# Kernel optimization log

Hardware: AMD Instinct MI355X
Metric: run time of the kernel (lower is better)

The kernel has to match this reference:

```python
import jax, jax.numpy as jnp
import numpy as np

N_NODES = 100000
N_EDGES = 1600000
D = 128


def gcn_conv(x, src, dst, ew, W, b, num_nodes):
    """PyG GCNConv: self-loops (weight 1), symmetric deg^{-1/2} normalization,
    linear transform (no bias) then scatter-add aggregation at dst, bias after."""
    loop = jnp.arange(num_nodes)
    s = jnp.concatenate([src, loop])
    d = jnp.concatenate([dst, loop])
    w = jnp.concatenate([ew, jnp.ones((num_nodes,), dtype=x.dtype)])
    deg = jax.ops.segment_sum(w, d, num_segments=num_nodes)
    dinv = jnp.where(deg > 0, jax.lax.rsqrt(deg), 0.0).astype(x.dtype)
    norm = dinv[s] * w * dinv[d]                      # [E+N]
    h = x @ W                                          # [N, out]
    msgs = h[s] * norm[:, None]                        # [E+N, out]
    return jax.ops.segment_sum(msgs, d, num_segments=num_nodes) + b


def setup_inputs() -> dict:
    key = jax.random.key(0)
    ks = jax.random.split(key, 7)
    x = jax.random.normal(ks[0], (N_NODES, D), dtype=jnp.float32)
    edge_index = jax.random.randint(ks[1], (2, N_EDGES), 0, N_NODES, dtype=jnp.int64)
    edge_weight = jax.random.uniform(ks[2], (N_EDGES,), dtype=jnp.float32)
    scale = 1.0 / np.sqrt(D)
    W1 = jax.random.normal(ks[3], (D, D), dtype=jnp.float32) * scale
    b1 = jax.random.normal(ks[4], (D,), dtype=jnp.float32) * 0.01
    W2 = jax.random.normal(ks[5], (D, D), dtype=jnp.float32) * scale
    b2 = jax.random.normal(ks[6], (D,), dtype=jnp.float32) * 0.01
    return {"x": x, "edge_index": edge_index, "edge_weight": edge_weight,
            "W1": W1, "b1": b1, "W2": W2, "b2": b2}


def reference(x, edge_index, edge_weight, W1, b1, W2, b2):
    src, dst = edge_index[0], edge_index[1]
    n = x.shape[0]
    h = gcn_conv(x, src, dst, edge_weight, W1, b1, n)
    h = jax.nn.relu(h)
    h = gcn_conv(h, src, dst, edge_weight, W2, b2, n)
    return jax.nn.relu(h)
```

## Files before the change

### kernel.cpp

```cpp
#include <hip/hip_runtime.h>

#define D 128
#define CAP 64
#define NCELL 391
#define BN2 256
#define CELLCAP 4608
#define BCAP 20
#define ABLK 512

typedef __attribute__((ext_vector_type(8))) short bf16x8;
typedef __attribute__((ext_vector_type(4))) float f32x4;

__device__ __forceinline__ ushort f2bf(float f) {
    uint u = __float_as_uint(f);
    return (ushort)((u + 0x7FFFu + ((u >> 16) & 1u)) >> 16);
}

__global__ __launch_bounds__(256) void k_prep(const float* __restrict__ W1,
                                              const float* __restrict__ W2,
                                              ushort* __restrict__ Wt1,
                                              ushort* __restrict__ Wt2,
                                              int* scnt) {
    int i = blockIdx.x * 256 + threadIdx.x;
    if (i < NCELL) scnt[i] = 0;
    if (i < 2 * D * D) {
        const float* W = (i < D * D) ? W1 : W2;
        ushort* Wt     = (i < D * D) ? Wt1 : Wt2;
        int j = i & (D * D - 1);
        int k = j >> 7, nn = j & 127;
        Wt[nn * D + k] = f2bf(W[k * D + nn]);
    }
}

__global__ __launch_bounds__(256) void k_bin(const int* __restrict__ src,
                                             const int* __restrict__ dst,
                                             const float* __restrict__ ew,
                                             int* scnt,
                                             uint2* __restrict__ rec, int nE, int epb) {
    __shared__ uint2 lrec[NCELL * BCAP];
    __shared__ int   bcnt[NCELL];
    __shared__ int   gbase[NCELL];
    const int tid = threadIdx.x;

    for (int i = tid; i < NCELL; i += 256) bcnt[i] = 0;
    __syncthreads();

    int e0 = blockIdx.x * epb;
    int e1 = min(e0 + epb, nE);
    for (int e = e0 + tid; e < e1; e += 256) {
        int d = dst[e];
        uint q = (uint)__float2int_rn(ew[e] * 32767.0f);
        uint2 r = make_uint2(((uint)src[e] << 15) | q, (uint)(d & (BN2 - 1)));
        int cell = d >> 8;
        int p = atomicAdd(&bcnt[cell], 1);
        if (p < BCAP) {
            lrec[cell * BCAP + p] = r;
        } else {
            int gp = atomicAdd(&scnt[cell], 1);
            if (gp < CELLCAP) rec[(size_t)cell * CELLCAP + gp] = r;
        }
    }
    __syncthreads();

    const int offs = (blockIdx.x * 97) % NCELL;

    for (int i = tid; i < NCELL; i += 256) {
        int cell = i + offs; if (cell >= NCELL) cell -= NCELL;
        int c = min(bcnt[cell], BCAP);
        gbase[cell] = (c > 0) ? atomicAdd(&scnt[cell], c) : 0;
    }
    __syncthreads();

    const int wave = tid >> 6, lane = tid & 63;
    for (int i = wave; i < NCELL; i += 4) {
        int cell = i + offs; if (cell >= NCELL) cell -= NCELL;
        int c = min(bcnt[cell], BCAP);
        if (lane < c)
            rec[(size_t)cell * CELLCAP + gbase[cell] + lane] = lrec[cell * BCAP + lane];
    }
}

__global__ __launch_bounds__(256) void k_build(const uint2* __restrict__ rec,
                                               const int* __restrict__ scnt,
                                               uint* __restrict__ bucket,
                                               int* __restrict__ cnt,
                                               float* __restrict__ dinv, int n) {
    __shared__ uint rows[BN2 * (CAP + 1)];
    __shared__ int  lcnt[BN2];
    const int tid = threadIdx.x;
    const int b   = blockIdx.x;

    lcnt[tid] = 0;
    __syncthreads();

    int c = min(scnt[b], CELLCAP);
    for (int i = tid; i < c; i += 256) {
        uint2 r = rec[(size_t)b * CELLCAP + i];
        int nl = (int)r.y;
        int p = atomicAdd(&lcnt[nl], 1);
        if (p < CAP) rows[nl * (CAP + 1) + p] = r.x;
    }
    __syncthreads();

    {
        int node = b * BN2 + tid;
        if (node < n) {
            int cc = min(lcnt[tid], CAP);
            float wsum = 0.f;
            for (int i = 0; i < cc; ++i)
                wsum += (float)(rows[tid * (CAP + 1) + i] & 32767u);
            dinv[node] = rsqrtf(1.0f + wsum * (1.0f / 32767.0f));
            cnt[node]  = cc;
        }
    }
    __syncthreads();

    for (int i = tid; i < BN2 * CAP; i += 256) {
        int nl = i >> 6, sl = i & (CAP - 1);
        int node = b * BN2 + nl;
        if (node < n) bucket[(size_t)node * CAP + sl] = rows[nl * (CAP + 1) + sl];
    }
}

template <bool IN_BF16>
__global__ __launch_bounds__(256) void k_gemm(const void* __restrict__ Xv,
                                              const ushort* __restrict__ Wt,
                                              ushort* __restrict__ H, int n) {
    __shared__ ushort Xs[64][136];
    __shared__ ushort Ws[128][136];
    const int tid  = threadIdx.x;
    const int row0 = blockIdx.x * 64;

#pragma unroll
    for (int p = 0; p < 8; ++p) {
        int f = (p * 256 + tid) * 8;
        int nn = f >> 7, kk = f & 127;
        *(uint4*)(&Ws[nn][kk]) = *(const uint4*)(Wt + f);
    }
    if (IN_BF16) {
        const ushort* X = (const ushort*)Xv;
#pragma unroll
        for (int p = 0; p < 4; ++p) {
            int f = (p * 256 + tid) * 8;
            int r = f >> 7, kk = f & 127;
            uint4 v = {0u, 0u, 0u, 0u};
            if (row0 + r < n) v = *(const uint4*)(X + (size_t)(row0 + r) * D + kk);
            *(uint4*)(&Xs[r][kk]) = v;
        }
    } else {
        const float* X = (const float*)Xv;
#pragma unroll
        for (int p = 0; p < 8; ++p) {
            int f = (p * 256 + tid) * 4;
            int r = f >> 7, kk = f & 127;
            float4 v = {0.f, 0.f, 0.f, 0.f};
            if (row0 + r < n) v = *(const float4*)(X + (size_t)(row0 + r) * D + kk);
            ushort4 o;
            o.x = f2bf(v.x); o.y = f2bf(v.y); o.z = f2bf(v.z); o.w = f2bf(v.w);
            *(ushort4*)(&Xs[r][kk]) = o;
        }
    }
    __syncthreads();

    const int lane = tid & 63;
    const int wave = tid >> 6;
    const int m    = lane & 15;
    const int quad = lane >> 4;
    const int rw   = wave * 16;

    f32x4 acc[8] = {};
#pragma unroll
    for (int kt = 0; kt < 4; ++kt) {
        int k0 = kt * 32 + quad * 8;
        bf16x8 a = *(const bf16x8*)(&Xs[rw + m][k0]);
#pragma unroll
        for (int t = 0; t < 8; ++t) {
            bf16x8 b = *(const bf16x8*)(&Ws[t * 16 + m][k0]);
            acc[t] = __builtin_amdgcn_mfma_f32_16x16x32_bf16(a, b, acc[t], 0, 0, 0);
        }
    }

#pragma unroll
    for (int t = 0; t < 8; ++t) {
#pragma unroll
        for (int r = 0; r < 4; ++r) {
            int row = row0 + rw + quad * 4 + r;
            if (row < n) H[(size_t)row * D + t * 16 + m] = f2bf(acc[t][r]);
        }
    }
}

template <bool OUT_BF16>
__global__ __launch_bounds__(256) void k_agg(const ushort* __restrict__ H,
                                             const int* __restrict__ cnt,
                                             const uint* __restrict__ bucket,
                                             const float* __restrict__ dinv,
                                             const float* __restrict__ bias,
                                             void* __restrict__ outv, int n) {
    int node = blockIdx.x * 4 + (threadIdx.x >> 6);
    if (node >= n) return;
    int lane = threadIdx.x & 63;
    const uint* Hu = (const uint*)H;
    const uint* row = bucket + (size_t)node * CAP;

    float di = dinv[node];
    float c0 = di * (1.0f / 32767.0f);
    uint hs = Hu[(size_t)node * 64 + lane];
    float accx = __uint_as_float(hs << 16) * (di * di);
    float accy = __uint_as_float(hs & 0xFFFF0000u) * (di * di);

    int c = cnt[node];
    int j = 0;
    for (; j + 3 < c; j += 4) {
        uint p0 = row[j],     p1 = row[j + 1];
        uint p2 = row[j + 2], p3 = row[j + 3];
        int s0 = p0 >> 15, s1 = p1 >> 15, s2 = p2 >> 15, s3 = p3 >> 15;
        uint h0 = Hu[(size_t)s0 * 64 + lane];
        uint h1 = Hu[(size_t)s1 * 64 + lane];
        uint h2 = Hu[(size_t)s2 * 64 + lane];
        uint h3 = Hu[(size_t)s3 * 64 + lane];
        float w0 = (float)(p0 & 32767u) * c0 * dinv[s0];
        float w1 = (float)(p1 & 32767u) * c0 * dinv[s1];
        float w2 = (float)(p2 & 32767u) * c0 * dinv[s2];
        float w3 = (float)(p3 & 32767u) * c0 * dinv[s3];
        accx += __uint_as_float(h0 << 16) * w0 + __uint_as_float(h1 << 16) * w1
              + __uint_as_float(h2 << 16) * w2 + __uint_as_float(h3 << 16) * w3;
        accy += __uint_as_float(h0 & 0xFFFF0000u) * w0 + __uint_as_float(h1 & 0xFFFF0000u) * w1
              + __uint_as_float(h2 & 0xFFFF0000u) * w2 + __uint_as_float(h3 & 0xFFFF0000u) * w3;
    }
    for (; j < c; ++j) {
        uint p = row[j];
        int s = p >> 15;
        uint h = Hu[(size_t)s * 64 + lane];
        float w = (float)(p & 32767u) * c0 * dinv[s];
        accx += __uint_as_float(h << 16) * w;
        accy += __uint_as_float(h & 0xFFFF0000u) * w;
    }

    float2 bv = *(const float2*)(bias + lane * 2);
    float rx = fmaxf(accx + bv.x, 0.f);
    float ry = fmaxf(accy + bv.y, 0.f);
    if (OUT_BF16) {
        uint o = (uint)f2bf(rx) | ((uint)f2bf(ry) << 16);
        ((uint*)outv)[(size_t)node * 64 + lane] = o;
    } else {
        float2 r; r.x = rx; r.y = ry;
        ((float2*)outv)[(size_t)node * 64 + lane] = r;
    }
}

extern "C" void kernel_launch(void* const* d_in, const int* in_sizes, int n_in,
                              void* d_out, int out_size, void* d_ws, size_t ws_size,
                              hipStream_t stream) {
    const float* x  = (const float*)d_in[0];
    const int*   ei = (const int*)d_in[1];
    const float* ew = (const float*)d_in[2];
    const float* W1 = (const float*)d_in[3];
    const float* b1 = (const float*)d_in[4];
    const float* W2 = (const float*)d_in[5];
    const float* b2 = (const float*)d_in[6];

    const int n  = in_sizes[0] / D;
    const int nE = in_sizes[2];
    const int* src = ei;
    const int* dst = ei + nE;

    float* out = (float*)d_out;

    uint2*  rec    = (uint2*)d_ws;
    uint*   bucket = (uint*)(rec + (size_t)NCELL * CELLCAP);
    ushort* Hbuf   = (ushort*)(bucket + (size_t)n * CAP);
    ushort* Abuf   = Hbuf + (size_t)n * D;
    ushort* Wt1    = Abuf + (size_t)n * D;
    ushort* Wt2    = Wt1 + D * D;
    float*  dinv   = (float*)(Wt2 + D * D);
    int*    cnt    = (int*)(dinv + n);
    int*    scnt   = cnt + n;

    const int epb      = (nE + ABLK - 1) / ABLK;
    const int nBlkWave = (n + 3) / 4;
    const int nBlkGemm = (n + 63) / 64;

    k_prep <<<128,   256, 0, stream>>>(W1, W2, Wt1, Wt2, scnt);
    k_bin  <<<ABLK,  256, 0, stream>>>(src, dst, ew, scnt, rec, nE, epb);
    k_build<<<NCELL, 256, 0, stream>>>(rec, scnt, bucket, cnt, dinv, n);

    k_gemm<false><<<nBlkGemm, 256, 0, stream>>>(x, Wt1, Hbuf, n);
    k_agg<true>  <<<nBlkWave, 256, 0, stream>>>(Hbuf, cnt, bucket, dinv, b1, Abuf, n);

    k_gemm<true> <<<nBlkGemm, 256, 0, stream>>>(Abuf, Wt2, Hbuf, n);
    k_agg<false> <<<nBlkWave, 256, 0, stream>>>(Hbuf, cnt, bucket, dinv, b2, out, n);
}
```

Baseline: 343.2 us.

## Precompute symmetric-normalized edge weights into buckets and simplify aggregation loop

Node degrees are now accumulated with global float atomics during binning, and a small kernel turns them into dinv. The build kernel then stores the fully normalized weight w*dinv[src]*dinv[dst], quantized to 15 bits, in each bucket entry, plus an explicit self-loop entry. The aggregation kernel therefore no longer gathers dinv per edge. Instead it reads bucket entries eight at a time with vector nontemporal loads, using zero-padded slots, and does plain FMAs. In exchange there are 1.6M global atomics, an extra launch, and more quantization error on small normalized weights.

```diff
diff --git a/kernel.cpp b/kernel.cpp
--- a/kernel.cpp
+++ b/kernel.cpp
@@ -10,6 +10,8 @@
 
 typedef __attribute__((ext_vector_type(8))) short bf16x8;
 typedef __attribute__((ext_vector_type(4))) float f32x4;
+typedef __attribute__((ext_vector_type(4))) uint  u32x4;
+typedef __attribute__((ext_vector_type(2))) float f32x2;
 
 __device__ __forceinline__ ushort f2bf(float f) {
     uint u = __float_as_uint(f);
@@ -20,7 +22,7 @@
                                               const float* __restrict__ W2,
                                               ushort* __restrict__ Wt1,
                                               ushort* __restrict__ Wt2,
-                                              int* scnt) {
+                                              int* scnt, float* __restrict__ deg, int n) {
     int i = blockIdx.x * 256 + threadIdx.x;
     if (i < NCELL) scnt[i] = 0;
     if (i < 2 * D * D) {
@@ -30,12 +32,13 @@
         int k = j >> 7, nn = j & 127;
         Wt[nn * D + k] = f2bf(W[k * D + nn]);
     }
+    if (i < n) deg[i] = 1.0f;
 }
 
 __global__ __launch_bounds__(256) void k_bin(const int* __restrict__ src,
                                              const int* __restrict__ dst,
                                              const float* __restrict__ ew,
-                                             int* scnt,
+                                             int* scnt, float* __restrict__ deg,
                                              uint2* __restrict__ rec, int nE, int epb) {
     __shared__ uint2 lrec[NCELL * BCAP];
     __shared__ int   bcnt[NCELL];
@@ -49,7 +52,9 @@
     int e1 = min(e0 + epb, nE);
     for (int e = e0 + tid; e < e1; e += 256) {
         int d = dst[e];
-        uint q = (uint)__float2int_rn(ew[e] * 32767.0f);
+        float w = ew[e];
+        atomicAdd(&deg[d], w);
+        uint q = (uint)__float2int_rn(w * 32767.0f);
         uint2 r = make_uint2(((uint)src[e] << 15) | q, (uint)(d & (BN2 - 1)));
         int cell = d >> 8;
         int p = atomicAdd(&bcnt[cell], 1);
@@ -80,13 +85,20 @@
     }
 }
 
+__global__ __launch_bounds__(256) void k_dinv(const float* __restrict__ deg,
+                                              float* __restrict__ dinv, int n) {
+    int i = blockIdx.x * 256 + threadIdx.x;
+    if (i < n) dinv[i] = rsqrtf(deg[i]);
+}
+
 __global__ __launch_bounds__(256) void k_build(const uint2* __restrict__ rec,
                                                const int* __restrict__ scnt,
+                                               const float* __restrict__ dinv,
                                                uint* __restrict__ bucket,
-                                               int* __restrict__ cnt,
-                                               float* __restrict__ dinv, int n) {
-    __shared__ uint rows[BN2 * (CAP + 1)];
-    __shared__ int  lcnt[BN2];
+                                               int* __restrict__ cnt, int n) {
+    __shared__ uint  rows[BN2 * (CAP + 1)];
+    __shared__ int   lcnt[BN2];
+    __shared__ float ldv[BN2];
     const int tid = threadIdx.x;
     const int b   = blockIdx.x;
 
@@ -98,27 +110,36 @@
         uint2 r = rec[(size_t)b * CELLCAP + i];
         int nl = (int)r.y;
         int p = atomicAdd(&lcnt[nl], 1);
-        if (p < CAP) rows[nl * (CAP + 1) + p] = r.x;
-    }
-    __syncthreads();
-
-    {
-        int node = b * BN2 + tid;
-        if (node < n) {
-            int cc = min(lcnt[tid], CAP);
-            float wsum = 0.f;
-            for (int i = 0; i < cc; ++i)
-                wsum += (float)(rows[tid * (CAP + 1) + i] & 32767u);
-            dinv[node] = rsqrtf(1.0f + wsum * (1.0f / 32767.0f));
-            cnt[node]  = cc;
-        }
-    }
+        if (p < CAP - 1) rows[nl * (CAP + 1) + p] = r.x;
+    }
+    __syncthreads();
+
+    int node = b * BN2 + tid;
+    float dv = (node < n) ? dinv[node] : 0.f;
+    ldv[tid] = dv;
+    int cc = min(lcnt[tid], CAP - 1);
+    lcnt[tid] = cc;
+    if (node < n) cnt[node] = cc + 1;
     __syncthreads();
 
     for (int i = tid; i < BN2 * CAP; i += 256) {
         int nl = i >> 6, sl = i & (CAP - 1);
-        int node = b * BN2 + nl;
-        if (node < n) bucket[(size_t)node * CAP + sl] = rows[nl * (CAP + 1) + sl];
+        int nd = b * BN2 + nl;
+        if (nd < n) {
+            int ce = lcnt[nl];
+            uint o;
+            if (sl < ce) {
+                uint r = rows[nl * (CAP + 1) + sl];
+                uint s = r >> 15;
+                float w = (float)(r & 32767u) * (1.0f / 32767.0f) * dinv[s] * ldv[nl];
+                o = (s << 15) | (uint)__float2int_rn(w * 32767.0f);
+            } else if (sl == ce) {
+                o = ((uint)nd << 15) | (uint)__float2int_rn(ldv[nl] * ldv[nl] * 32767.0f);
+            } else {
+                o = 0u;
+            }
+            bucket[(size_t)b * (BN2 * CAP) + i] = o;
+        }
     }
 }
 
@@ -194,58 +215,39 @@
 __global__ __launch_bounds__(256) void k_agg(const ushort* __restrict__ H,
                                              const int* __restrict__ cnt,
                                              const uint* __restrict__ bucket,
-                                             const float* __restrict__ dinv,
                                              const float* __restrict__ bias,
                                              void* __restrict__ outv, int n) {
     int node = blockIdx.x * 4 + (threadIdx.x >> 6);
     if (node >= n) return;
     int lane = threadIdx.x & 63;
-    const uint* Hu = (const uint*)H;
-    const uint* row = bucket + (size_t)node * CAP;
-
-    float di = dinv[node];
-    float c0 = di * (1.0f / 32767.0f);
-    uint hs = Hu[(size_t)node * 64 + lane];
-    float accx = __uint_as_float(hs << 16) * (di * di);
-    float accy = __uint_as_float(hs & 0xFFFF0000u) * (di * di);
+    const uint*  Hu   = (const uint*)H;
+    const u32x4* row4 = (const u32x4*)(bucket + (size_t)node * CAP);
 
     int c = cnt[node];
-    int j = 0;
-    for (; j + 3 < c; j += 4) {
-        uint p0 = row[j],     p1 = row[j + 1];
-        uint p2 = row[j + 2], p3 = row[j + 3];
-        int s0 = p0 >> 15, s1 = p1 >> 15, s2 = p2 >> 15, s3 = p3 >> 15;
-        uint h0 = Hu[(size_t)s0 * 64 + lane];
-        uint h1 = Hu[(size_t)s1 * 64 + lane];
-        uint h2 = Hu[(size_t)s2 * 64 + lane];
-        uint h3 = Hu[(size_t)s3 * 64 + lane];
-        float w0 = (float)(p0 & 32767u) * c0 * dinv[s0];
-        float w1 = (float)(p1 & 32767u) * c0 * dinv[s1];
-        float w2 = (float)(p2 & 32767u) * c0 * dinv[s2];
-        float w3 = (float)(p3 & 32767u) * c0 * dinv[s3];
-        accx += __uint_as_float(h0 << 16) * w0 + __uint_as_float(h1 << 16) * w1
-              + __uint_as_float(h2 << 16) * w2 + __uint_as_float(h3 << 16) * w3;
-        accy += __uint_as_float(h0 & 0xFFFF0000u) * w0 + __uint_as_float(h1 & 0xFFFF0000u) * w1
-              + __uint_as_float(h2 & 0xFFFF0000u) * w2 + __uint_as_float(h3 & 0xFFFF0000u) * w3;
-    }
-    for (; j < c; ++j) {
-        uint p = row[j];
-        int s = p >> 15;
-        uint h = Hu[(size_t)s * 64 + lane];
-        float w = (float)(p & 32767u) * c0 * dinv[s];
-        accx += __uint_as_float(h << 16) * w;
-        accy += __uint_as_float(h & 0xFFFF0000u) * w;
-    }
-
-    float2 bv = *(const float2*)(bias + lane * 2);
+    float accx = 0.f, accy = 0.f;
+    for (int j = 0; j < c; j += 8) {
+        u32x4 pa = __builtin_nontemporal_load(row4 + (j >> 2));
+        u32x4 pb = __builtin_nontemporal_load(row4 + (j >> 2) + 1);
+#pragma unroll
+        for (int t = 0; t < 8; ++t) {
+            uint p   = (t < 4) ? pa[t] : pb[t - 4];
+            uint off = ((p >> 9) & 0x007FFFC0u) | (uint)lane;
+            uint h   = Hu[off];
+            float w  = (float)(p & 32767u) * (1.0f / 32767.0f);
+            accx = fmaf(__uint_as_float(h << 16), w, accx);
+            accy = fmaf(__uint_as_float(h & 0xFFFF0000u), w, accy);
+        }
+    }
+
+    f32x2 bv = *(const f32x2*)(bias + lane * 2);
     float rx = fmaxf(accx + bv.x, 0.f);
     float ry = fmaxf(accy + bv.y, 0.f);
     if (OUT_BF16) {
         uint o = (uint)f2bf(rx) | ((uint)f2bf(ry) << 16);
         ((uint*)outv)[(size_t)node * 64 + lane] = o;
     } else {
-        float2 r; r.x = rx; r.y = ry;
-        ((float2*)outv)[(size_t)node * 64 + lane] = r;
+        f32x2 r; r.x = rx; r.y = ry;
+        __builtin_nontemporal_store(r, (f32x2*)outv + (size_t)node * 64 + lane);
     }
 }
 
@@ -276,18 +278,21 @@
     float*  dinv   = (float*)(Wt2 + D * D);
     int*    cnt    = (int*)(dinv + n);
     int*    scnt   = cnt + n;
+    float*  deg    = (float*)bucket;
 
     const int epb      = (nE + ABLK - 1) / ABLK;
+    const int nBlkNode = (n + 255) / 256;
     const int nBlkWave = (n + 3) / 4;
     const int nBlkGemm = (n + 63) / 64;
 
-    k_prep <<<128,   256, 0, stream>>>(W1, W2, Wt1, Wt2, scnt);
-    k_bin  <<<ABLK,  256, 0, stream>>>(src, dst, ew, scnt, rec, nE, epb);
-    k_build<<<NCELL, 256, 0, stream>>>(rec, scnt, bucket, cnt, dinv, n);
+    k_prep <<<nBlkNode, 256, 0, stream>>>(W1, W2, Wt1, Wt2, scnt, deg, n);
+    k_bin  <<<ABLK,     256, 0, stream>>>(src, dst, ew, scnt, deg, rec, nE, epb);
+    k_dinv <<<nBlkNode, 256, 0, stream>>>(deg, dinv, n);
+    k_build<<<NCELL,    256, 0, stream>>>(rec, scnt, dinv, bucket, cnt, n);
 
     k_gemm<false><<<nBlkGemm, 256, 0, stream>>>(x, Wt1, Hbuf, n);
-    k_agg<true>  <<<nBlkWave, 256, 0, stream>>>(Hbuf, cnt, bucket, dinv, b1, Abuf, n);
+    k_agg<true>  <<<nBlkWave, 256, 0, stream>>>(Hbuf, cnt, bucket, b1, Abuf, n);
 
     k_gemm<true> <<<nBlkGemm, 256, 0, stream>>>(Abuf, Wt2, Hbuf, n);
-    k_agg<false> <<<nBlkWave, 256, 0, stream>>>(Hbuf, cnt, bucket, dinv, b2, out, n);
-}
+    k_agg<false> <<<nBlkWave, 256, 0, stream>>>(Hbuf, cnt, bucket, b2, out, n);
+}
```

Measured after the change: 419.9 us. +22.3%, slower.
